# Kernel optimization log

Measured on AMD Instinct MI355X. Metric: run time of the kernel, lower is better.

The kernel has to match this reference:

```python
import jax, jax.numpy as jnp
import numpy as np

TEMP = 0.07
NUM_CLASSES = 4

def setup_inputs() -> dict:
    key = jax.random.key(0)
    k1, k2 = jax.random.split(key)
    features_in = jax.random.normal(k1, (4, 64, 2048), dtype=jnp.float32)
    labels_in = jax.random.randint(k2, (4, 2048), 0, NUM_CLASSES, dtype=jnp.int64)
    return {"features_in": features_in, "labels_in": labels_in}

def reference(features_in, labels_in):
    B, C, N = features_in.shape
    M = B * N
    # torch .view(C, B*N): row-major reinterpret of contiguous [B,C,N]
    feats = features_in.reshape(C, M).T            # [M, C]
    labels = labels_in.reshape(-1)                 # [M]

    # per-class keep probability: min(750/(count+1), 1), gathered by label
    counts = jnp.bincount(labels, length=NUM_CLASSES)
    keep_p = jnp.minimum(750.0 / (counts.astype(jnp.float32) + 1.0), 1.0)
    p = keep_p[labels]                             # [M]
    sel = jax.random.bernoulli(jax.random.key(42), p)  # [M] bool, stochastic subsample

    # L2 normalize rows; original divides by norms of already-normalized rows (==1)
    nv = feats / jnp.linalg.norm(feats, axis=1, keepdims=True)
    sim = nv @ nv.T                                # [M, M] cosine similarities
    dp = jnp.exp(sim / TEMP)
    dp = dp * (1.0 - jnp.eye(M, dtype=dp.dtype))   # zero the diagonal

    same = labels[:, None] == labels[None, :]
    pair = sel[:, None] & sel[None, :]             # both points kept
    pos = jnp.sum(jnp.where(same & pair, dp, 0.0), axis=1)
    neg = jnp.sum(jnp.where((~same) & pair, dp, 0.0), axis=1)

    frac = pos / (pos + neg)
    per = -jnp.log(jnp.where(sel, frac, 1.0))      # guard unselected rows
    n_sel = jnp.maximum(jnp.sum(sel), 1)
    loss = jnp.sum(jnp.where(sel, per, 0.0)) / n_sel
    return loss
```

## Files before the change

### kernel.cpp

```cpp
#include <hip/hip_runtime.h>
#include <hip/hip_bf16.h>

#define M_TOT 8192
#define NCLS 4
#define NSEL_CAP 4096
#define NT 64

typedef __attribute__((ext_vector_type(8)))  short short8v;
typedef __attribute__((ext_vector_type(16))) float f32x16;

__device__ __forceinline__ unsigned int rotl32(unsigned int x, unsigned int r) {
    return (x << r) | (x >> (32u - r));
}

__device__ __forceinline__ uint2 threefry_pair_key42(unsigned int j) {
    const unsigned int ks0 = 0u;
    const unsigned int ks1 = 42u;
    const unsigned int ks2 = 0x1BD11BDAu ^ 0u ^ 42u;
    unsigned int x0 = j + ks0;
    unsigned int x1 = (j + 4096u) + ks1;
#define TF_RND(r) { x0 += x1; x1 = rotl32(x1, (r)); x1 ^= x0; }
    TF_RND(13u) TF_RND(15u) TF_RND(26u) TF_RND(6u)
    x0 += ks1; x1 += ks2 + 1u;
    TF_RND(17u) TF_RND(29u) TF_RND(16u) TF_RND(24u)
    x0 += ks2; x1 += ks0 + 2u;
    TF_RND(13u) TF_RND(15u) TF_RND(26u) TF_RND(6u)
    x0 += ks0; x1 += ks1 + 3u;
    TF_RND(17u) TF_RND(29u) TF_RND(16u) TF_RND(24u)
    x0 += ks1; x1 += ks2 + 4u;
    TF_RND(13u) TF_RND(15u) TF_RND(26u) TF_RND(6u)
    x0 += ks2; x1 += ks0 + 5u;
#undef TF_RND
    return make_uint2(x0, x1);
}

__device__ __forceinline__ float bits_to_unit(unsigned int bits) {
    return __uint_as_float((bits >> 9) | 0x3F800000u) - 1.0f;
}

__device__ __forceinline__ unsigned short f2bf(float x) {
    const unsigned int u = __float_as_uint(x);
    return (unsigned short)((u + 0x7FFFu + ((u >> 16) & 1u)) >> 16);
}
__device__ __forceinline__ float bf2f(unsigned short b) {
    return __uint_as_float(((unsigned int)b) << 16);
}

__global__ __launch_bounds__(256) void select_norm_kernel(
        const float* __restrict__ features,
        const int* __restrict__ labels,
        int* __restrict__ nsel_g,
        int* __restrict__ lab_sel,
        unsigned short* __restrict__ nv_hi,
        unsigned short* __restrict__ nv_lo,
        float* __restrict__ pos,
        float* __restrict__ neg) {
    __shared__ int   hist[NCLS];
    __shared__ float keepp[NCLS];
    __shared__ int   wtot[4];
    __shared__ int   lds_m[NSEL_CAP];
    const int t = threadIdx.x, b = blockIdx.x;
    const int lane = t & 63, w = t >> 6;

    const int gid = b * 256 + t;
    if (gid < NSEL_CAP) { pos[gid] = 0.0f; neg[gid] = 0.0f; }
    if (t < NCLS) hist[t] = 0;
    __syncthreads();

    {
        const int m0 = t * 32;
        int c0 = 0, c1 = 0, c2 = 0, c3 = 0;
        for (int r = 0; r < 32; ++r) {
            const int lab = labels[m0 + r];
            c0 += (lab == 0); c1 += (lab == 1); c2 += (lab == 2); c3 += (lab == 3);
        }
        int cc[4] = {c0, c1, c2, c3};
        #pragma unroll
        for (int cls = 0; cls < NCLS; ++cls) {
            int v = cc[cls];
            for (int off = 32; off > 0; off >>= 1) v += __shfl_down(v, off, 64);
            if (lane == 0) atomicAdd(&hist[cls], v);
        }
    }
    __syncthreads();
    if (t < NCLS) keepp[t] = fminf(750.0f / ((float)hist[t] + 1.0f), 1.0f);
    __syncthreads();

    const int jb = t * 16;
    unsigned int flags = 0u;
    int cnt = 0;
    for (int r = 0; r < 16; ++r) {
        const uint2 bb = threefry_pair_key42((unsigned int)(jb + r));
        if (bits_to_unit(bb.x) < keepp[labels[jb + r]])        { flags |= 1u << r;        ++cnt; }
        if (bits_to_unit(bb.y) < keepp[labels[jb + r + 4096]]) { flags |= 1u << (16 + r); ++cnt; }
    }
    int x = cnt;
    #pragma unroll
    for (int off = 1; off < 64; off <<= 1) {
        const int y = __shfl_up(x, off, 64);
        if (lane >= off) x += y;
    }
    if (lane == 63) wtot[w] = x;
    const int excl = x - cnt;
    __syncthreads();
    int base = excl;
    for (int w2 = 0; w2 < w; ++w2) base += wtot[w2];
    const int nsel = wtot[0] + wtot[1] + wtot[2] + wtot[3];
    if (b == 0 && t == 0) *nsel_g = nsel;
    for (int r = 0; r < 16; ++r) {
        if (flags & (1u << r))        lds_m[base++] = jb + r;
        if (flags & (1u << (16 + r))) lds_m[base++] = jb + r + 4096;
    }
    __syncthreads();

    const int p  = b * 32 + (t >> 3);
    const int kg = t & 7;
    if (p >= nsel) return;
    const int m = lds_m[p];
    if (kg == 0) lab_sel[p] = labels[m];
    float v[8];
    float ss = 0.0f;
    #pragma unroll
    for (int q = 0; q < 8; ++q) {
        v[q] = features[(kg * 8 + q) * M_TOT + m];
        ss += v[q] * v[q];
    }
    ss += __shfl_xor(ss, 1, 8);
    ss += __shfl_xor(ss, 2, 8);
    ss += __shfl_xor(ss, 4, 8);
    const float rn = rsqrtf(ss);
    unsigned short hs[8], ls[8];
    #pragma unroll
    for (int q = 0; q < 8; ++q) {
        const float xx = v[q] * rn;
        const unsigned short h = f2bf(xx);
        hs[q] = h;
        ls[q] = f2bf(xx - bf2f(h));
    }
    const int ofs = (p << 6) + kg * 8;
    *(uint4*)&nv_hi[ofs] = *(const uint4*)hs;
    *(uint4*)&nv_lo[ofs] = *(const uint4*)ls;
}

#define EXP2_SCALE 20.609929155556605f

__global__ __launch_bounds__(256, 4) void pair_kernel(
        const unsigned short* __restrict__ nv_hi,
        const unsigned short* __restrict__ nv_lo,
        const int* __restrict__ lab_sel,
        const int* __restrict__ nsel_g,
        float* __restrict__ pos,
        float* __restrict__ neg) {
    const int nsel = *nsel_g;
    const int it = blockIdx.y, jt = blockIdx.x;
    const int i0 = it * 64, j0 = jt * 64;
    if (i0 >= nsel || j0 >= nsel) return;

    __shared__ __align__(16) unsigned short frags[2][2][8][64][8];
    __shared__ int La[64], Lb[64];

    const int t = threadIdx.x;
    const int wave = t >> 6, lane = t & 63;

    #pragma unroll
    for (int it8 = 0; it8 < 8; ++it8) {
        const int slot = it8 * 256 + t;
        const int side  = slot >> 10;
        const int plane = (slot >> 9) & 1;
        const int c     = (slot >> 6) & 7;
        const int row   = slot & 63;
        const unsigned short* src = plane ? nv_lo : nv_hi;
        const int basep = (side ? j0 : i0) + row;
        const uint4 v = *(const uint4*)&src[(basep << 6) + c * 8];
        *(uint4*)&((unsigned short*)frags)[slot * 8] = v;
    }
    if (t < 64)       La[t]      = lab_sel[i0 + t];
    else if (t < 128) Lb[t - 64] = lab_sel[j0 + t - 64];
    __syncthreads();

    const int qi = (wave >> 1) * 32, qj = (wave & 1) * 32;
    const int half = lane >> 5, l31 = lane & 31;
    const int ra = qi + l31, rb = qj + l31;

    f32x16 acc;
    #pragma unroll
    for (int r = 0; r < 16; ++r) acc[r] = 0.0f;

    #pragma unroll
    for (int s = 0; s < 4; ++s) {
        const int c = 2 * s + half;
        const short8v ah = *(const short8v*)&frags[0][0][c][ra][0];
        const short8v al = *(const short8v*)&frags[0][1][c][ra][0];
        const short8v bh = *(const short8v*)&frags[1][0][c][rb][0];
        const short8v bl = *(const short8v*)&frags[1][1][c][rb][0];
        acc = __builtin_amdgcn_mfma_f32_32x32x16_bf16(ah, bh, acc, 0, 0, 0);
        acc = __builtin_amdgcn_mfma_f32_32x32x16_bf16(ah, bl, acc, 0, 0, 0);
        acc = __builtin_amdgcn_mfma_f32_32x32x16_bf16(al, bh, acc, 0, 0, 0);
    }

    const int colL = qj + l31;
    const int jg = j0 + colL;
    const int Lj = Lb[colL];
    float cp = 0.0f, cn = 0.0f;
    #pragma unroll
    for (int r = 0; r < 16; ++r) {
        const int rowL = qi + (r & 3) + 8 * (r >> 2) + 4 * half;
        const int ig = i0 + rowL;
        const bool valid = (ig < nsel) && (jg < nsel) && (ig != jg);
        const float d = valid ? exp2f(acc[r] * EXP2_SCALE) : 0.0f;
        if (La[rowL] == Lj) cp += d; else cn += d;
    }
    cp += __shfl_xor(cp, 32, 64);
    cn += __shfl_xor(cn, 32, 64);
    if (half == 0 && jg < nsel) {
        atomicAdd(&pos[jg], cp);
        atomicAdd(&neg[jg], cn);
    }
}

__global__ void loss_kernel(const float* __restrict__ pos,
                            const float* __restrict__ neg,
                            const int* __restrict__ nsel_g,
                            float* __restrict__ out) {
    const int nsel = *nsel_g;
    float s = 0.0f;
    for (int i = threadIdx.x; i < nsel; i += 256) {
        const float fr = pos[i] / (pos[i] + neg[i]);
        s += -logf(fr);
    }
    __shared__ float red[256];
    red[threadIdx.x] = s;
    __syncthreads();
    for (int off = 128; off > 0; off >>= 1) {
        if (threadIdx.x < off) red[threadIdx.x] += red[threadIdx.x + off];
        __syncthreads();
    }
    if (threadIdx.x == 0) out[0] = red[0] / (float)(nsel > 0 ? nsel : 1);
}

extern "C" void kernel_launch(void* const* d_in, const int* in_sizes, int n_in,
                              void* d_out, int out_size, void* d_ws, size_t ws_size,
                              hipStream_t stream) {
    const float* features = (const float*)d_in[0];
    const int*   labels   = (const int*)d_in[1];
    float*       out      = (float*)d_out;
    char*        ws       = (char*)d_ws;

    int*   nsel_g   = (int*)(ws);
    int*   lab_sel  = (int*)(ws + 1024);
    float* pos      = (float*)(ws + 1024 + 16384);
    float* neg      = pos + NSEL_CAP;
    unsigned short* nv_hi = (unsigned short*)(ws + 1024 + 16384 + 32768);
    unsigned short* nv_lo = nv_hi + NSEL_CAP * 64;

    select_norm_kernel<<<128, 256, 0, stream>>>(features, labels, nsel_g, lab_sel,
                                                nv_hi, nv_lo, pos, neg);
    pair_kernel<<<dim3(NT, NT), 256, 0, stream>>>(nv_hi, nv_lo, lab_sel, nsel_g, pos, neg);
    loss_kernel<<<1, 256, 0, stream>>>(pos, neg, nsel_g, out);
}
```

Before: 87.73 us.

## Exploit similarity symmetry by computing only upper-triangular tile pairs

Launches only the upper-triangular set of 64x64 tiles, decoding the tile pair from a linear block index with a sqrt-based inverse. Each off-diagonal tile adds its contributions both to column sums (as before) and, through wave shuffle reductions, to row sums, which roughly halves the MFMA and exp work. The cost is extra shuffle reductions and per-row atomics in every off-diagonal tile, plus index-decoding arithmetic.

```diff
diff --git a/kernel.cpp b/kernel.cpp
--- a/kernel.cpp
+++ b/kernel.cpp
@@ -5,6 +5,7 @@
 #define NCLS 4
 #define NSEL_CAP 4096
 #define NT 64
+#define NTRI (NT * (NT + 1) / 2)
 
 typedef __attribute__((ext_vector_type(8)))  short short8v;
 typedef __attribute__((ext_vector_type(16))) float f32x16;
@@ -152,9 +153,14 @@
         float* __restrict__ pos,
         float* __restrict__ neg) {
     const int nsel = *nsel_g;
-    const int it = blockIdx.y, jt = blockIdx.x;
+    const int q = blockIdx.x;
+    int it = (int)((129.0f - sqrtf(16641.0f - 8.0f * (float)q)) * 0.5f);
+    while (it > 0 && q < it * (129 - it) / 2) --it;
+    while (q >= (it + 1) * (128 - it) / 2) ++it;
+    const int jt = it + (q - it * (129 - it) / 2);
     const int i0 = it * 64, j0 = jt * 64;
     if (i0 >= nsel || j0 >= nsel) return;
+    const bool diag = (it == jt);
 
     __shared__ __align__(16) unsigned short frags[2][2][8][64][8];
     __shared__ int La[64], Lb[64];
@@ -202,19 +208,42 @@
     const int jg = j0 + colL;
     const int Lj = Lb[colL];
     float cp = 0.0f, cn = 0.0f;
+    float rp[16], rn2[16];
     #pragma unroll
     for (int r = 0; r < 16; ++r) {
         const int rowL = qi + (r & 3) + 8 * (r >> 2) + 4 * half;
         const int ig = i0 + rowL;
         const bool valid = (ig < nsel) && (jg < nsel) && (ig != jg);
         const float d = valid ? exp2f(acc[r] * EXP2_SCALE) : 0.0f;
-        if (La[rowL] == Lj) cp += d; else cn += d;
+        const bool match = (La[rowL] == Lj);
+        cp += match ? d : 0.0f;
+        cn += match ? 0.0f : d;
+        rp[r]  = match ? d : 0.0f;
+        rn2[r] = match ? 0.0f : d;
     }
     cp += __shfl_xor(cp, 32, 64);
     cn += __shfl_xor(cn, 32, 64);
     if (half == 0 && jg < nsel) {
         atomicAdd(&pos[jg], cp);
         atomicAdd(&neg[jg], cn);
+    }
+    if (!diag) {
+        #pragma unroll
+        for (int r = 0; r < 16; ++r) {
+            float p = rp[r], n = rn2[r];
+            #pragma unroll
+            for (int off = 16; off > 0; off >>= 1) {
+                p += __shfl_xor(p, off, 32);
+                n += __shfl_xor(n, off, 32);
+            }
+            if (l31 == 0) {
+                const int ig = i0 + qi + (r & 3) + 8 * (r >> 2) + 4 * half;
+                if (ig < nsel) {
+                    atomicAdd(&pos[ig], p);
+                    atomicAdd(&neg[ig], n);
+                }
+            }
+        }
     }
 }
 
@@ -255,6 +284,6 @@
 
     select_norm_kernel<<<128, 256, 0, stream>>>(features, labels, nsel_g, lab_sel,
                                                 nv_hi, nv_lo, pos, neg);
-    pair_kernel<<<dim3(NT, NT), 256, 0, stream>>>(nv_hi, nv_lo, lab_sel, nsel_g, pos, neg);
+    pair_kernel<<<NTRI, 256, 0, stream>>>(nv_hi, nv_lo, lab_sel, nsel_g, pos, neg);
     loss_kernel<<<1, 256, 0, stream>>>(pos, neg, nsel_g, out);
 }
```

Result: slower. 104.0 us (+18.5%).

## Load pair-kernel tiles with global_load_lds using a chunk-major nv layout

Applied to the files above, without the earlier changes.

Stores the normalized hi/lo bf16 vectors in a [plane][chunk][point][8] layout, so each wave's 64 lanes read one contiguous 1 KiB run for a chunk. The pair kernel then fills its LDS tile with global_load_lds direct-to-LDS copies instead of going through registers. This is meant to cut register staging and VGPR pressure in the tile load. It depends on the builtin's 16-byte form and its LDS addressing being correct on this target, and there is no explicit wait beyond the existing syncthreads.

```diff
diff --git a/kernel.cpp b/kernel.cpp
--- a/kernel.cpp
+++ b/kernel.cpp
@@ -8,6 +8,14 @@
 
 typedef __attribute__((ext_vector_type(8)))  short short8v;
 typedef __attribute__((ext_vector_type(16))) float f32x16;
+
+__device__ __forceinline__ void async_copy16(const void* gsrc, void* ldst) {
+#if defined(__HIP_DEVICE_COMPILE__)
+    __builtin_amdgcn_global_load_lds(
+        (const __attribute__((address_space(1))) void*)gsrc,
+        (__attribute__((address_space(3))) void*)ldst, 16, 0, 0);
+#endif
+}
 
 __device__ __forceinline__ unsigned int rotl32(unsigned int x, unsigned int r) {
     return (x << r) | (x >> (32u - r));
@@ -46,13 +54,14 @@
     return __uint_as_float(((unsigned int)b) << 16);
 }
 
+#define NV_OFS(plane, c, p) (((((plane) << 3) + (c)) << 12) + (p))
+
 __global__ __launch_bounds__(256) void select_norm_kernel(
         const float* __restrict__ features,
         const int* __restrict__ labels,
         int* __restrict__ nsel_g,
         int* __restrict__ lab_sel,
-        unsigned short* __restrict__ nv_hi,
-        unsigned short* __restrict__ nv_lo,
+        unsigned short* __restrict__ nv,
         float* __restrict__ pos,
         float* __restrict__ neg) {
     __shared__ int   hist[NCLS];
@@ -137,16 +146,14 @@
         hs[q] = h;
         ls[q] = f2bf(xx - bf2f(h));
     }
-    const int ofs = (p << 6) + kg * 8;
-    *(uint4*)&nv_hi[ofs] = *(const uint4*)hs;
-    *(uint4*)&nv_lo[ofs] = *(const uint4*)ls;
+    *(uint4*)&nv[NV_OFS(0, kg, p) * 8] = *(const uint4*)hs;
+    *(uint4*)&nv[NV_OFS(1, kg, p) * 8] = *(const uint4*)ls;
 }
 
 #define EXP2_SCALE 20.609929155556605f
 
 __global__ __launch_bounds__(256, 4) void pair_kernel(
-        const unsigned short* __restrict__ nv_hi,
-        const unsigned short* __restrict__ nv_lo,
+        const unsigned short* __restrict__ nv,
         const int* __restrict__ lab_sel,
         const int* __restrict__ nsel_g,
         float* __restrict__ pos,
@@ -164,15 +171,13 @@
 
     #pragma unroll
     for (int it8 = 0; it8 < 8; ++it8) {
-        const int slot = it8 * 256 + t;
-        const int side  = slot >> 10;
-        const int plane = (slot >> 9) & 1;
-        const int c     = (slot >> 6) & 7;
-        const int row   = slot & 63;
-        const unsigned short* src = plane ? nv_lo : nv_hi;
-        const int basep = (side ? j0 : i0) + row;
-        const uint4 v = *(const uint4*)&src[(basep << 6) + c * 8];
-        *(uint4*)&((unsigned short*)frags)[slot * 8] = v;
+        const int combo = it8 * 4 + wave;
+        const int side  = combo >> 4;
+        const int plane = (combo >> 3) & 1;
+        const int c     = combo & 7;
+        const int base0 = (side ? j0 : i0);
+        async_copy16(&nv[NV_OFS(plane, c, base0 + lane) * 8],
+                     &frags[side][plane][c][lane][0]);
     }
     if (t < 64)       La[t]      = lab_sel[i0 + t];
     else if (t < 128) Lb[t - 64] = lab_sel[j0 + t - 64];
@@ -250,11 +255,10 @@
     int*   lab_sel  = (int*)(ws + 1024);
     float* pos      = (float*)(ws + 1024 + 16384);
     float* neg      = pos + NSEL_CAP;
-    unsigned short* nv_hi = (unsigned short*)(ws + 1024 + 16384 + 32768);
-    unsigned short* nv_lo = nv_hi + NSEL_CAP * 64;
+    unsigned short* nv = (unsigned short*)(ws + 1024 + 16384 + 32768);
 
     select_norm_kernel<<<128, 256, 0, stream>>>(features, labels, nsel_g, lab_sel,
-                                                nv_hi, nv_lo, pos, neg);
-    pair_kernel<<<dim3(NT, NT), 256, 0, stream>>>(nv_hi, nv_lo, lab_sel, nsel_g, pos, neg);
+                                                nv, pos, neg);
+    pair_kernel<<<dim3(NT, NT), 256, 0, stream>>>(nv, lab_sel, nsel_g, pos, neg);
     loss_kernel<<<1, 256, 0, stream>>>(pos, neg, nsel_g, out);
 }
```

After: 82.71 us, median of 2. 1.06x faster.
